# Kernel tuning notes

Hardware: AMD Instinct MI355X
Metric: run time of the kernel (lower is better)

The kernel has to match this reference:

```python
import jax, jax.numpy as jnp
import numpy as np
from jax import lax

B, T, D, U = 64, 512, 1024, 1024
INIT_SCALE = 0.05  # keras 'uniform' initializer: U(-0.05, 0.05)


def setup_inputs() -> dict:
    key = jax.random.key(0)
    kx, kw, ku = jax.random.split(key, 3)
    x = jax.random.normal(kx, (B, T, D), dtype=jnp.float32)
    kernel = jax.random.uniform(kw, (D, U), dtype=jnp.float32,
                                minval=-INIT_SCALE, maxval=INIT_SCALE)
    recurrent_kernel = jax.random.uniform(ku, (U, U), dtype=jnp.float32,
                                          minval=-INIT_SCALE, maxval=INIT_SCALE)
    return {"x": x, "kernel": kernel, "recurrent_kernel": recurrent_kernel}


def reference(x, kernel, recurrent_kernel):
    # h_t = x_t @ W + h_{t-1} @ U, h_0 = 0; return last h (return_sequences=False)
    # Precompute the input projection for all timesteps in one big GEMM.
    xs = jnp.einsum('btd,du->btu', x, kernel)          # [B, T, U]
    h0 = jnp.zeros((x.shape[0], recurrent_kernel.shape[0]), dtype=x.dtype)

    def step(h, xt):
        h = xt + h @ recurrent_kernel                   # [B, U]
        return h, None

    h_last, _ = lax.scan(step, h0, jnp.swapaxes(xs, 0, 1))  # scan over T
    return h_last                                       # [B, U]
```

## Files before the change

kernel.cpp:

```cpp
#include <hip/hip_runtime.h>
#include <hip/hip_bf16.h>

typedef __attribute__((ext_vector_type(4))) float f32x4;
typedef __attribute__((ext_vector_type(8))) short bf16x8;
typedef __attribute__((ext_vector_type(4))) short s16x4;

#define SLOT (1024 * 1024)

__device__ __forceinline__ short f2bfs(float f) {
  __hip_bfloat16 h = __float2bfloat16(f);
  union { __hip_bfloat16 h; short s; } u; u.h = h;
  return u.s;
}
__device__ __forceinline__ float bf2fs(short s) {
  union { unsigned u; float f; } v; v.u = ((unsigned)(unsigned short)s) << 16;
  return v.f;
}

__device__ __forceinline__ void gload16(void* l, const void* g) {
  __builtin_amdgcn_global_load_lds(
      (const __attribute__((address_space(1))) unsigned int*)g,
      (__attribute__((address_space(3))) unsigned int*)l, 16, 0, 0);
}

template<int RM>
__device__ __forceinline__ int rmap(int R) {
  return (RM == 0) ? R
       : (RM == 3) ? (((R & 63) << 9) | ((R >> 6) << 2))
                   : (((R >> 6) << 7) | (R & 63));
}

template<int ADD, int OUT>
__device__ __forceinline__ void epi128(
    f32x4 (&acc)[4][4], void* __restrict__ Cp, int ldc,
    const short* __restrict__ AddP,
    int row0, int col0, int M, int wave, int lane) {
  const int wm = wave >> 1, wn = wave & 1;
  const int l16 = lane & 15;
  #pragma unroll
  for (int m = 0; m < 4; ++m) {
    #pragma unroll
    for (int n = 0; n < 4; ++n) {
      const int grow0 = row0 + wm * 64 + m * 16 + ((lane >> 4) << 2);
      const int gcol  = col0 + wn * 64 + n * 16 + l16;
      #pragma unroll
      for (int r = 0; r < 4; ++r) {
        const int R = grow0 + r;
        if (R < M) {
          float val = acc[m][n][r];
          if (ADD == 2) {
            int ar = (((R >> 6) << 7) | (R & 63)) + 64;
            val += bf2fs(AddP[(size_t)ar * 1024 + gcol]);
          }
          if (OUT == 0) ((short*)Cp)[(size_t)R * ldc + gcol] = f2bfs(val);
          else          ((float*)Cp)[(size_t)R * ldc + gcol] = val;
        }
      }
    }
  }
}

struct TileAddr {
  const short *a0, *a1, *b0, *b1;
  int dA0, dA1, dB0, dB1;
  int offA[4], offB[4];
};
template<int RM>
__device__ __forceinline__ TileAddr mk_addr(
    const short* A, int lda, const short* BT, int ldb,
    int row0, int col0, int tid, int wave, int lane) {
  TileAddr t;
  const int wm = wave >> 1, wn = wave & 1;
  const int l16 = lane & 15, kg = lane >> 4;
  const int r0 = tid >> 2, g0 = tid & 3;
  const int gs0 = g0 ^ ((r0 >> 1) & 3);
  const int r1 = r0 + 64;
  const int gs1 = g0 ^ ((r1 >> 1) & 3);
  t.a0 = A + (size_t)rmap<RM>(row0 + r0) * lda + gs0 * 8;
  t.a1 = A + (size_t)rmap<RM>(row0 + r1) * lda + gs1 * 8;
  t.b0 = BT + (size_t)(col0 + r0) * ldb + gs0 * 8;
  t.b1 = BT + (size_t)(col0 + r1) * ldb + gs1 * 8;
  t.dA0 = tid * 16; t.dA1 = t.dA0 + 4096;
  t.dB0 = 8192 + tid * 16; t.dB1 = t.dB0 + 4096;
  #pragma unroll
  for (int m = 0; m < 4; ++m) {
    int row = wm * 64 + m * 16 + l16;
    t.offA[m] = (row * 4 + (kg ^ ((row >> 1) & 3))) * 16;
  }
  #pragma unroll
  for (int n = 0; n < 4; ++n) {
    int c = wn * 64 + n * 16 + l16;
    t.offB[n] = 8192 + (c * 4 + (kg ^ ((c >> 1) & 3))) * 16;
  }
  return t;
}
__device__ __forceinline__ void stage_to(const TileAddr& ta, char* buf, int ko) {
  gload16(buf + ta.dA0, ta.a0 + ko); gload16(buf + ta.dA1, ta.a1 + ko);
  gload16(buf + ta.dB0, ta.b0 + ko); gload16(buf + ta.dB1, ta.b1 + ko);
}
__device__ __forceinline__ void compute_step(
    const TileAddr& ta, const char* buf, f32x4 (&acc)[4][4]) {
  bf16x8 af[4], bfr[4];
  #pragma unroll
  for (int m = 0; m < 4; ++m) af[m] = *(const bf16x8*)(buf + ta.offA[m]);
  #pragma unroll
  for (int n = 0; n < 4; ++n) bfr[n] = *(const bf16x8*)(buf + ta.offB[n]);
  __builtin_amdgcn_s_setprio(1);
  #pragma unroll
  for (int m = 0; m < 4; ++m)
    #pragma unroll
    for (int n = 0; n < 4; ++n)
      acc[m][n] = __builtin_amdgcn_mfma_f32_16x16x32_bf16(af[m], bfr[n], acc[m][n], 0, 0, 0);
  __builtin_amdgcn_s_setprio(0);
}
template<int RM>
__device__ __forceinline__ void gemm128_d4(
    char* lds, f32x4 (&acc)[4][4],
    const short* __restrict__ A, int lda,
    const short* __restrict__ BT, int ldb,
    int row0, int col0, int nkt, int tid, int wave, int lane) {
  TileAddr ta = mk_addr<RM>(A, lda, BT, ldb, row0, col0, tid, wave, lane);
  #pragma unroll
  for (int p = 0; p < 4; ++p)
    stage_to(ta, lds + p * 16384, p * 32);
  int bufc = 0, bufn = 4;
  for (int t = 0; t < nkt; ++t) {
    const int w = nkt - 1 - t;
    if (w >= 3)      { asm volatile("s_waitcnt vmcnt(12)" ::: "memory"); }
    else if (w == 2) { asm volatile("s_waitcnt vmcnt(8)" ::: "memory"); }
    else if (w == 1) { asm volatile("s_waitcnt vmcnt(4)" ::: "memory"); }
    else             { asm volatile("s_waitcnt vmcnt(0)" ::: "memory"); }
    __builtin_amdgcn_s_barrier();
    asm volatile("" ::: "memory");
    if (t + 4 < nkt) stage_to(ta, lds + bufn * 16384, (t + 4) * 32);
    compute_step(ta, lds + bufc * 16384, acc);
    bufc = (bufc == 4) ? 0 : bufc + 1;
    bufn = (bufn == 4) ? 0 : bufn + 1;
  }
}
__device__ __forceinline__ void run_unit_d4(char* lds,
    const short* A, const short* BT, short* C, int ldc,
    int tile, int tid, int wave, int lane) {
  f32x4 acc[4][4] = {};
  int row0 = (tile >> 3) * 128, col0 = (tile & 7) * 128;
  gemm128_d4<0>(lds, acc, A, 1024, BT, 1024, row0, col0, 32, tid, wave, lane);
  epi128<0, 0>(acc, C, ldc, nullptr, row0, col0, 1024, wave, lane);
}

template<int RM>
__device__ __forceinline__ void gemm8ph(
    char* lds, f32x4 (&acc)[4][4],
    const short* __restrict__ A, int lda,
    const short* __restrict__ BT, int ldb,
    int row0, int col0, int nkt, int tid, int wave, int lane) {
  const int wm = wave >> 1, wn = wave & 1;
  const int l16 = lane & 15, kg = (lane >> 4) & 3;

  const short* aP[2][2];
  #pragma unroll
  for (int l = 0; l < 2; ++l) {
    int G = l * 512 + tid;
    int rp = G >> 3, gs = (G & 7) ^ (rp & 7);
    #pragma unroll
    for (int h = 0; h < 2; ++h)
      aP[l][h] = A + (size_t)rmap<RM>(row0 + h * 128 + rp) * lda + gs * 8;
  }
  const short* bP[2];
  {
    int rp = tid >> 3, gs = (tid & 7) ^ (rp & 7);
    #pragma unroll
    for (int h = 0; h < 2; ++h)
      bP[h] = BT + (size_t)(col0 + h * 64 + rp) * ldb + gs * 8;
  }

  int offA[4][2], offB[4][2];
  #pragma unroll
  for (int m = 0; m < 4; ++m) {
    int rp = (wm & 1) * 64 + m * 16 + l16;
    #pragma unroll
    for (int ks = 0; ks < 2; ++ks) {
      int gsrc = ks * 4 + kg;
      offA[m][ks] = (wm >> 1) * 16384 + (rp * 8 + (gsrc ^ (rp & 7))) * 16;
    }
  }
  #pragma unroll
  for (int n = 0; n < 4; ++n) {
    int rp = n * 16 + l16;
    #pragma unroll
    for (int ks = 0; ks < 2; ++ks) {
      int gsrc = ks * 4 + kg;
      offB[n][ks] = wn * 8192 + (rp * 8 + (gsrc ^ (rp & 7))) * 16;
    }
  }

  auto SA = [&](int kt, int ad_t, int h) {
    char* dst = lds + ad_t * 32768 + h * 16384 + tid * 16;
    gload16(dst,        aP[0][h] + kt * 64);
    gload16(dst + 8192, aP[1][h] + kt * 64);
  };
  auto SB = [&](int kt, int h) {
    gload16(lds + 98304 + (kt & 1) * 16384 + h * 8192 + tid * 16,
            bP[h] + kt * 64);
  };

  SA(0, 0, 0); SA(0, 0, 1);
  SB(0, 0); SB(0, 1);
  SA(1, 1, 0); SA(1, 1, 1);
  SB(1, 0); SB(1, 1);

  bf16x8 bR[4][2];
  int ad = 0;
  for (int kt = 0; kt < nkt; ++kt) {
    char* baseA = lds + ad * 32768;
    char* baseB = lds + 98304 + (kt & 1) * 16384;
    const int ad2 = (ad >= 1) ? ad - 1 : 2;
    if (kt == nkt - 1) { asm volatile("s_waitcnt vmcnt(0)" ::: "memory"); }
    else               { asm volatile("s_waitcnt vmcnt(6)" ::: "memory"); }
    __builtin_amdgcn_s_barrier();
    __builtin_amdgcn_sched_barrier(0);
    {
      #pragma unroll
      for (int n = 0; n < 4; ++n)
        #pragma unroll
        for (int ks = 0; ks < 2; ++ks)
          bR[n][ks] = *(const bf16x8*)(baseB + offB[n][ks]);
      bf16x8 aR[2][2];
      #pragma unroll
      for (int mm = 0; mm < 2; ++mm)
        #pragma unroll
        for (int ks = 0; ks < 2; ++ks)
          aR[mm][ks] = *(const bf16x8*)(baseA + offA[mm][ks]);
      if (kt + 2 < nkt) { SA(kt + 2, ad2, 0); SA(kt + 2, ad2, 1); }
      __builtin_amdgcn_s_setprio(1);
      #pragma unroll
      for (int mm = 0; mm < 2; ++mm)
        #pragma unroll
        for (int n = 0; n < 4; ++n)
          #pragma unroll
          for (int ks = 0; ks < 2; ++ks)
            acc[mm][n] = __builtin_amdgcn_mfma_f32_16x16x32_bf16(
                aR[mm][ks], bR[n][ks], acc[mm][n], 0, 0, 0);
      __builtin_amdgcn_s_setprio(0);
    }
    __builtin_amdgcn_s_barrier();
    __builtin_amdgcn_sched_barrier(0);
    {
      bf16x8 aR[2][2];
      #pragma unroll
      for (int mm = 0; mm < 2; ++mm)
        #pragma unroll
        for (int ks = 0; ks < 2; ++ks)
          aR[mm][ks] = *(const bf16x8*)(baseA + offA[2 + mm][ks]);
      if (kt + 2 < nkt) { SB(kt + 2, 0); SB(kt + 2, 1); }
      __builtin_amdgcn_s_setprio(1);
      #pragma unroll
      for (int mm = 0; mm < 2; ++mm)
        #pragma unroll
        for (int n = 0; n < 4; ++n)
          #pragma unroll
          for (int ks = 0; ks < 2; ++ks)
            acc[2 + mm][n] = __builtin_amdgcn_mfma_f32_16x16x32_bf16(
                aR[mm][ks], bR[n][ks], acc[2 + mm][n], 0, 0, 0);
      __builtin_amdgcn_s_setprio(0);
    }
    ad = (ad == 2) ? 0 : ad + 1;
  }
}

__device__ __forceinline__ void run_unit8(char* lds,
    const short* A, const short* BT, short* C, int ldc,
    int tile, int tid, int wave, int lane) {
  f32x4 acc[4][4] = {};
  int row0 = (tile >> 3) * 256, col0 = (tile & 7) * 128;
  gemm8ph<0>(lds, acc, A, 1024, BT, 1024, row0, col0, 16, tid, wave, lane);
  epi128<0, 0>(acc, C, ldc, nullptr, row0, col0, 1024, wave, lane);
}


__global__ __launch_bounds__(256) void k_prep_tc(
    const float* __restrict__ W, const float* __restrict__ Uf,
    short* __restrict__ BTcat, short* __restrict__ slab) {
  __shared__ float tf[32][36];
  int b = blockIdx.x, t = threadIdx.x;
  if (b < 2048) {
    const float* src = (b < 1024) ? W : Uf;
    int bb = b & 1023;
    int i0 = (bb >> 5) * 32, j0 = (bb & 31) * 32;
    int r = t >> 3, c = (t & 7) * 4;
    *(f32x4*)&tf[r][c] = *(const f32x4*)(src + (size_t)(i0 + r) * 1024 + j0 + c);
    __syncthreads();
    s16x4 o;
    o.x = f2bfs(tf[c + 0][r]); o.y = f2bfs(tf[c + 1][r]);
    o.z = f2bfs(tf[c + 2][r]); o.w = f2bfs(tf[c + 3][r]);
    if (b < 1024)
      *(s16x4*)(BTcat + (size_t)(j0 + r) * 4096 + 3072 + i0 + c) = o;
    else
      *(s16x4*)(slab + (size_t)(j0 + r) * 1024 + i0 + c) = o;
  } else {
    int q = b - 2048;
    const float* src = (q < 512) ? Uf : W;
    short* dst = slab + (size_t)((q < 512) ? 9 : 17) * SLOT;
    int qq = q & 511;
    size_t base = (size_t)qq * 2048 + (size_t)t * 8;
    f32x4 a = *(const f32x4*)(src + base);
    f32x4 c2 = *(const f32x4*)(src + base + 4);
    bf16x8 o;
    o[0] = f2bfs(a.x);  o[1] = f2bfs(a.y);  o[2] = f2bfs(a.z);  o[3] = f2bfs(a.w);
    o[4] = f2bfs(c2.x); o[5] = f2bfs(c2.y); o[6] = f2bfs(c2.z); o[7] = f2bfs(c2.w);
    *(bf16x8*)(dst + base) = o;
  }
}

template<int PH>
__global__ __launch_bounds__(512) void k_fuse(
    const float* __restrict__ X, short* __restrict__ XB,
    short* slab, short* BTcat) {
  __shared__ __align__(16) char lds[131072];
  int tid = threadIdx.x;
  int b = blockIdx.x;
  short* s = slab;
  if (b < 128) {
    int wave = tid >> 6, lane = tid & 63;
    int u = b >> 5, q = b & 31;
    if (PH == 0) {
      if (u == 0)
        run_unit8(lds, s, s + (size_t)9 * SLOT, s + (size_t)1 * SLOT, 1024, q, tid, wave, lane);
      else if (u == 1)
        run_unit8(lds, s + (size_t)9 * SLOT, s, s + (size_t)10 * SLOT, 1024, q, tid, wave, lane);
      else if (u == 2)
        run_unit8(lds, s, s + (size_t)17 * SLOT, BTcat + 2048, 4096, q, tid, wave, lane);
      else
        run_unit8(lds, s + (size_t)17 * SLOT, s, s + (size_t)16 * SLOT, 1024, q, tid, wave, lane);
    } else {
      if (u == 0)
        run_unit8(lds, s + (size_t)1 * SLOT, s + (size_t)17 * SLOT, BTcat + 1024, 4096, q, tid, wave, lane);
      else if (u == 1)
        run_unit8(lds, s + (size_t)1 * SLOT, s + (size_t)16 * SLOT, BTcat, 4096, q, tid, wave, lane);
      else if (u == 2)
        run_unit8(lds, s + (size_t)1 * SLOT, s + (size_t)10 * SLOT, s + (size_t)2 * SLOT, 1024, q, tid, wave, lane);
      else
        run_unit8(lds, s + (size_t)10 * SLOT, s + (size_t)1 * SLOT, s + (size_t)11 * SLOT, 1024, q, tid, wave, lane);
    }
  } else {
    size_t base = ((size_t)(b - 128 + PH * 2048)) * 8192;
    #pragma unroll
    for (int i = 0; i < 4; ++i) {
      size_t idx = base + (size_t)i * 2048 + (size_t)tid * 4;
      f32x4 v = *(const f32x4*)(X + idx);
      s16x4 o;
      o.x = f2bfs(v.x); o.y = f2bfs(v.y); o.z = f2bfs(v.z); o.w = f2bfs(v.w);
      *(s16x4*)(XB + idx) = o;
    }
  }
}

__global__ __launch_bounds__(512) void k_big(
    const short* __restrict__ XB, const short* __restrict__ BTcat,
    short* __restrict__ FA) {
  __shared__ __align__(16) char lds[131072];
  int tid = threadIdx.x, wave = tid >> 6, lane = tid & 63;
  int c = blockIdx.x;
  int c2 = (c & 7) * 32 + (c >> 3);
  f32x4 acc[4][4] = {};
  int row0 = (c2 >> 3) * 256, col0 = (c2 & 7) * 128;
  gemm8ph<3>(lds, acc, XB, 1024, BTcat, 4096, row0, col0, 64, tid, wave, lane);
  epi128<0, 0>(acc, FA, 1024, nullptr, row0, col0, 8192, wave, lane);
}

template<int OUT>
__global__ __launch_bounds__(256) void k_lvl(
    const short* __restrict__ Fin, const short* __restrict__ PT,
    void* __restrict__ Fout, int M, int nComb,
    const short* __restrict__ sA0, const short* __restrict__ sB0, short* __restrict__ sC0,
    const short* __restrict__ sA1, const short* __restrict__ sB1, short* __restrict__ sC1) {
  __shared__ __align__(16) char lds[81920];
  int tid = threadIdx.x, wave = tid >> 6, lane = tid & 63;
  int b = blockIdx.x;
  if (b < nComb) {
    f32x4 acc[4][4] = {};
    int row0 = (b >> 3) * 128, col0 = (b & 7) * 128;
    gemm128_d4<2>(lds, acc, Fin, 1024, PT, 1024, row0, col0, 32, tid, wave, lane);
    epi128<2, OUT>(acc, Fout, 1024, Fin, row0, col0, M, wave, lane);
  } else {
    int q = b - nComb;
    const short* sa = (q < 64) ? sA0 : sA1;
    const short* sb = (q < 64) ? sB0 : sB1;
    short* sc = (q < 64) ? sC0 : sC1;
    run_unit_d4(lds, sa, sb, sc, 1024, q & 63, tid, wave, lane);
  }
}

extern "C" void kernel_launch(void* const* d_in, const int* in_sizes, int n_in,
                              void* d_out, int out_size, void* d_ws, size_t ws_size,
                              hipStream_t stream) {
  const float* X = (const float*)d_in[0];
  const float* W = (const float*)d_in[1];
  const float* U = (const float*)d_in[2];
  float* outp = (float*)d_out;

  char* ws = (char*)d_ws;
  short* XB    = (short*)ws;
  short* FB    = (short*)ws;
  short* BTcat = (short*)(ws + ((size_t)64 << 20));
  short* slab  = (short*)(ws + ((size_t)72 << 20));
  short* FA    = (short*)(ws + ((size_t)108 << 20));
  auto sl = [&](int i) { return slab + (size_t)i * SLOT; };

  k_prep_tc<<<3072, 256, 0, stream>>>(W, U, BTcat, slab);
  k_fuse<0><<<2176, 512, 0, stream>>>(X, XB, slab, BTcat);
  k_fuse<1><<<2176, 512, 0, stream>>>(X, XB, slab, BTcat);
  k_big<<<256, 512, 0, stream>>>(XB, BTcat, FA);

  k_lvl<0><<<384, 256, 0, stream>>>(FA, sl(2), FB, 4096, 256,
                                    sl(2), sl(11), sl(3), sl(11), sl(2), sl(12));
  k_lvl<0><<<256, 256, 0, stream>>>(FB, sl(3), FA, 2048, 128,
                                    sl(3), sl(12), sl(4), sl(12), sl(3), sl(13));
  k_lvl<0><<<192, 256, 0, stream>>>(FA, sl(4), FB, 1024, 64,
                                    sl(4), sl(13), sl(5), sl(13), sl(4), sl(14));
  k_lvl<0><<<160, 256, 0, stream>>>(FB, sl(5), FA, 512, 32,
                                    sl(5), sl(14), sl(6), sl(14), sl(5), sl(15));
  k_lvl<0><<<144, 256, 0, stream>>>(FA, sl(6), FB, 256, 16,
                                    sl(6), sl(15), sl(7), sl(15), sl(6), sl(16));
  k_lvl<0><<<72, 256, 0, stream>>>(FB, sl(7), FA, 128, 8,
                                   sl(7), sl(16), sl(8), nullptr, nullptr, nullptr);
  k_lvl<1><<<8, 256, 0, stream>>>(FA, sl(8), outp, 64, 8,
                                  nullptr, nullptr, nullptr, nullptr, nullptr, nullptr);
}
```

Measured before the change: 299.8 us.

## Switch level kernels to 256x128 tiles with 8-wave 8-phase GEMM pipeline

The per-level combine kernels move from 4-wave 128x128 tiles with a 4-deep buffer pipeline to 8-wave 512-thread blocks that reuse the gemm8ph path from k_big, with 256-row tiles and 128 KB of LDS. Block counts for the combine and side-product work are halved to match. The aim is better operand reuse per tile and fewer blocks per level. The cost is fewer blocks on the small late levels, which lowers occupancy and parallelism. It depends on gemm8ph and run_unit8 supporting the new nkt and row mapping.

```diff
diff --git a/kernel.cpp b/kernel.cpp
--- a/kernel.cpp
+++ b/kernel.cpp
@@ -58,93 +58,6 @@
       }
     }
   }
-}
-
-struct TileAddr {
-  const short *a0, *a1, *b0, *b1;
-  int dA0, dA1, dB0, dB1;
-  int offA[4], offB[4];
-};
-template<int RM>
-__device__ __forceinline__ TileAddr mk_addr(
-    const short* A, int lda, const short* BT, int ldb,
-    int row0, int col0, int tid, int wave, int lane) {
-  TileAddr t;
-  const int wm = wave >> 1, wn = wave & 1;
-  const int l16 = lane & 15, kg = lane >> 4;
-  const int r0 = tid >> 2, g0 = tid & 3;
-  const int gs0 = g0 ^ ((r0 >> 1) & 3);
-  const int r1 = r0 + 64;
-  const int gs1 = g0 ^ ((r1 >> 1) & 3);
-  t.a0 = A + (size_t)rmap<RM>(row0 + r0) * lda + gs0 * 8;
-  t.a1 = A + (size_t)rmap<RM>(row0 + r1) * lda + gs1 * 8;
-  t.b0 = BT + (size_t)(col0 + r0) * ldb + gs0 * 8;
-  t.b1 = BT + (size_t)(col0 + r1) * ldb + gs1 * 8;
-  t.dA0 = tid * 16; t.dA1 = t.dA0 + 4096;
-  t.dB0 = 8192 + tid * 16; t.dB1 = t.dB0 + 4096;
-  #pragma unroll
-  for (int m = 0; m < 4; ++m) {
-    int row = wm * 64 + m * 16 + l16;
-    t.offA[m] = (row * 4 + (kg ^ ((row >> 1) & 3))) * 16;
-  }
-  #pragma unroll
-  for (int n = 0; n < 4; ++n) {
-    int c = wn * 64 + n * 16 + l16;
-    t.offB[n] = 8192 + (c * 4 + (kg ^ ((c >> 1) & 3))) * 16;
-  }
-  return t;
-}
-__device__ __forceinline__ void stage_to(const TileAddr& ta, char* buf, int ko) {
-  gload16(buf + ta.dA0, ta.a0 + ko); gload16(buf + ta.dA1, ta.a1 + ko);
-  gload16(buf + ta.dB0, ta.b0 + ko); gload16(buf + ta.dB1, ta.b1 + ko);
-}
-__device__ __forceinline__ void compute_step(
-    const TileAddr& ta, const char* buf, f32x4 (&acc)[4][4]) {
-  bf16x8 af[4], bfr[4];
-  #pragma unroll
-  for (int m = 0; m < 4; ++m) af[m] = *(const bf16x8*)(buf + ta.offA[m]);
-  #pragma unroll
-  for (int n = 0; n < 4; ++n) bfr[n] = *(const bf16x8*)(buf + ta.offB[n]);
-  __builtin_amdgcn_s_setprio(1);
-  #pragma unroll
-  for (int m = 0; m < 4; ++m)
-    #pragma unroll
-    for (int n = 0; n < 4; ++n)
-      acc[m][n] = __builtin_amdgcn_mfma_f32_16x16x32_bf16(af[m], bfr[n], acc[m][n], 0, 0, 0);
-  __builtin_amdgcn_s_setprio(0);
-}
-template<int RM>
-__device__ __forceinline__ void gemm128_d4(
-    char* lds, f32x4 (&acc)[4][4],
-    const short* __restrict__ A, int lda,
-    const short* __restrict__ BT, int ldb,
-    int row0, int col0, int nkt, int tid, int wave, int lane) {
-  TileAddr ta = mk_addr<RM>(A, lda, BT, ldb, row0, col0, tid, wave, lane);
-  #pragma unroll
-  for (int p = 0; p < 4; ++p)
-    stage_to(ta, lds + p * 16384, p * 32);
-  int bufc = 0, bufn = 4;
-  for (int t = 0; t < nkt; ++t) {
-    const int w = nkt - 1 - t;
-    if (w >= 3)      { asm volatile("s_waitcnt vmcnt(12)" ::: "memory"); }
-    else if (w == 2) { asm volatile("s_waitcnt vmcnt(8)" ::: "memory"); }
-    else if (w == 1) { asm volatile("s_waitcnt vmcnt(4)" ::: "memory"); }
-    else             { asm volatile("s_waitcnt vmcnt(0)" ::: "memory"); }
-    __builtin_amdgcn_s_barrier();
-    asm volatile("" ::: "memory");
-    if (t + 4 < nkt) stage_to(ta, lds + bufn * 16384, (t + 4) * 32);
-    compute_step(ta, lds + bufc * 16384, acc);
-    bufc = (bufc == 4) ? 0 : bufc + 1;
-    bufn = (bufn == 4) ? 0 : bufn + 1;
-  }
-}
-__device__ __forceinline__ void run_unit_d4(char* lds,
-    const short* A, const short* BT, short* C, int ldc,
-    int tile, int tid, int wave, int lane) {
-  f32x4 acc[4][4] = {};
-  int row0 = (tile >> 3) * 128, col0 = (tile & 7) * 128;
-  gemm128_d4<0>(lds, acc, A, 1024, BT, 1024, row0, col0, 32, tid, wave, lane);
-  epi128<0, 0>(acc, C, ldc, nullptr, row0, col0, 1024, wave, lane);
 }
 
 template<int RM>
@@ -368,25 +281,25 @@
 }
 
 template<int OUT>
-__global__ __launch_bounds__(256) void k_lvl(
+__global__ __launch_bounds__(512) void k_lvl8(
     const short* __restrict__ Fin, const short* __restrict__ PT,
     void* __restrict__ Fout, int M, int nComb,
     const short* __restrict__ sA0, const short* __restrict__ sB0, short* __restrict__ sC0,
     const short* __restrict__ sA1, const short* __restrict__ sB1, short* __restrict__ sC1) {
-  __shared__ __align__(16) char lds[81920];
+  __shared__ __align__(16) char lds[131072];
   int tid = threadIdx.x, wave = tid >> 6, lane = tid & 63;
   int b = blockIdx.x;
   if (b < nComb) {
     f32x4 acc[4][4] = {};
-    int row0 = (b >> 3) * 128, col0 = (b & 7) * 128;
-    gemm128_d4<2>(lds, acc, Fin, 1024, PT, 1024, row0, col0, 32, tid, wave, lane);
+    int row0 = (b >> 3) * 256, col0 = (b & 7) * 128;
+    gemm8ph<2>(lds, acc, Fin, 1024, PT, 1024, row0, col0, 16, tid, wave, lane);
     epi128<2, OUT>(acc, Fout, 1024, Fin, row0, col0, M, wave, lane);
   } else {
     int q = b - nComb;
-    const short* sa = (q < 64) ? sA0 : sA1;
-    const short* sb = (q < 64) ? sB0 : sB1;
-    short* sc = (q < 64) ? sC0 : sC1;
-    run_unit_d4(lds, sa, sb, sc, 1024, q & 63, tid, wave, lane);
+    const short* sa = (q < 32) ? sA0 : sA1;
+    const short* sb = (q < 32) ? sB0 : sB1;
+    short* sc = (q < 32) ? sC0 : sC1;
+    run_unit8(lds, sa, sb, sc, 1024, q & 31, tid, wave, lane);
   }
 }
 
@@ -411,18 +324,18 @@
   k_fuse<1><<<2176, 512, 0, stream>>>(X, XB, slab, BTcat);
   k_big<<<256, 512, 0, stream>>>(XB, BTcat, FA);
 
-  k_lvl<0><<<384, 256, 0, stream>>>(FA, sl(2), FB, 4096, 256,
-                                    sl(2), sl(11), sl(3), sl(11), sl(2), sl(12));
-  k_lvl<0><<<256, 256, 0, stream>>>(FB, sl(3), FA, 2048, 128,
-                                    sl(3), sl(12), sl(4), sl(12), sl(3), sl(13));
-  k_lvl<0><<<192, 256, 0, stream>>>(FA, sl(4), FB, 1024, 64,
+  k_lvl8<0><<<192, 512, 0, stream>>>(FA, sl(2), FB, 4096, 128,
+                                     sl(2), sl(11), sl(3), sl(11), sl(2), sl(12));
+  k_lvl8<0><<<128, 512, 0, stream>>>(FB, sl(3), FA, 2048, 64,
+                                     sl(3), sl(12), sl(4), sl(12), sl(3), sl(13));
+  k_lvl8<0><<<96, 512, 0, stream>>>(FA, sl(4), FB, 1024, 32,
                                     sl(4), sl(13), sl(5), sl(13), sl(4), sl(14));
-  k_lvl<0><<<160, 256, 0, stream>>>(FB, sl(5), FA, 512, 32,
+  k_lvl8<0><<<80, 512, 0, stream>>>(FB, sl(5), FA, 512, 16,
                                     sl(5), sl(14), sl(6), sl(14), sl(5), sl(15));
-  k_lvl<0><<<144, 256, 0, stream>>>(FA, sl(6), FB, 256, 16,
+  k_lvl8<0><<<72, 512, 0, stream>>>(FA, sl(6), FB, 256, 8,
                                     sl(6), sl(15), sl(7), sl(15), sl(6), sl(16));
-  k_lvl<0><<<72, 256, 0, stream>>>(FB, sl(7), FA, 128, 8,
-                                   sl(7), sl(16), sl(8), nullptr, nullptr, nullptr);
-  k_lvl<1><<<8, 256, 0, stream>>>(FA, sl(8), outp, 64, 8,
-                                  nullptr, nullptr, nullptr, nullptr, nullptr, nullptr);
-}
+  k_lvl8<0><<<40, 512, 0, stream>>>(FB, sl(7), FA, 128, 8,
+                                    sl(7), sl(16), sl(8), nullptr, nullptr, nullptr);
+  k_lvl8<1><<<8, 512, 0, stream>>>(FA, sl(8), outp, 64, 8,
+                                   nullptr, nullptr, nullptr, nullptr, nullptr, nullptr);
+}
```

Result: slower. 312.6 us (+4.3%).
